# Kernel optimization log

Hardware: AMD Instinct MI355X
Metric: run time of the kernel (lower is better)

The kernel has to match this reference:

```python
import jax, jax.numpy as jnp
import numpy as np

B, C, T, N = 8, 64, 24, 512
H = 2
D = C // H  # 32
NEG = -1e9
LN_EPS = 1e-5


def setup_inputs() -> dict:
    key = jax.random.key(0)
    ks = jax.random.split(key, 8)
    s = 1.0 / np.sqrt(C)
    return {
        "x": jax.random.normal(ks[0], (B, C, T, N), jnp.float32),
        "gso": jax.random.randint(ks[1], (N, N), 0, 2, jnp.int32),
        "Wq": jax.random.normal(ks[2], (C, C), jnp.float32) * s,
        "Wk": jax.random.normal(ks[3], (C, C), jnp.float32) * s,
        "Wv": jax.random.normal(ks[4], (C, C), jnp.float32) * s,
        "a_src": jax.random.normal(ks[5], (H, D), jnp.float32) * s,
        "a_dst": jax.random.normal(ks[6], (H, D), jnp.float32) * s,
        "gamma": jnp.ones((C,), jnp.float32),
        "beta": jnp.zeros((C,), jnp.float32),
    }


def reference(x, gso, Wq, Wk, Wv, a_src, a_dst, gamma, beta):
    # x: (B, C, T, N) -> (M, N, C) with M = B*T
    xr = jnp.transpose(x, (0, 2, 3, 1)).reshape(B * T, N, C)
    # torch Linear: y = x @ W.T ; split heads -> (M, N, H, D)
    Q = jnp.einsum('mnc,dc->mnd', xr, Wq).reshape(B * T, N, H, D)
    K = jnp.einsum('mnc,dc->mnd', xr, Wk).reshape(B * T, N, H, D)
    V = jnp.einsum('mnc,dc->mnd', xr, Wv).reshape(B * T, N, H, D)
    # additive GAT scores: s_ij = leaky_relu(<q_i, a_src> + <k_j, a_dst>)
    s_src = jnp.einsum('mnhd,hd->mhn', Q, a_src)  # (M, H, N)
    s_dst = jnp.einsum('mnhd,hd->mhn', K, a_dst)  # (M, H, N)
    scores = s_src[:, :, :, None] + s_dst[:, :, None, :]  # (M, H, N, N)
    scores = jax.nn.leaky_relu(scores, negative_slope=0.2)
    mask = jnp.where(gso == 0, jnp.float32(NEG), jnp.float32(0.0))  # (N, N)
    scores = scores + mask[None, None, :, :]
    attn = jax.nn.softmax(scores, axis=-1)  # dropout is identity in eval
    out = jnp.einsum('mhij,mjhd->mihd', attn, V).reshape(B * T, N, C)
    # LayerNorm over channels
    mu = jnp.mean(out, axis=-1, keepdims=True)
    var = jnp.var(out, axis=-1, keepdims=True)
    out = (out - mu) * jax.lax.rsqrt(var + LN_EPS) * gamma + beta
    # (M, N, C) -> (B, C, T, N)
    return jnp.transpose(out.reshape(B, T, N, C), (0, 3, 1, 2))
```

## Files before the change

kernel.cpp:

```cpp
#include <hip/hip_runtime.h>


#define NB 8
#define NC 64
#define NT 24
#define NN 512
#define NM 192
#define LOG2E 1.44269504088896f
#define NEGBIG -1.0e9f

typedef float f32x4 __attribute__((ext_vector_type(4)));
typedef short bf16x8 __attribute__((ext_vector_type(8)));
typedef int   i32x4 __attribute__((ext_vector_type(4)));
typedef unsigned int u32;
typedef u32 u32x2 __attribute__((ext_vector_type(2)));

#ifndef __has_builtin
#define __has_builtin(x) 0
#endif

__device__ __forceinline__ float fast_exp2(float x) {
#if __has_builtin(__builtin_amdgcn_exp2f)
    return __builtin_amdgcn_exp2f(x);
#else
    return exp2f(x);
#endif
}

__device__ __forceinline__ unsigned short f2bf(float f) {
    union { float f; unsigned int u; } v; v.f = f;
    unsigned int u = v.u;
    u += 0x7fffu + ((u >> 16) & 1u);
    return (unsigned short)(u >> 16);
}

__device__ __forceinline__ float bf2f(unsigned short s) {
    union { unsigned int u; float f; } v;
    v.u = ((unsigned int)s) << 16;
    return v.f;
}

#define VT_IDX(h,k,qq,dt,dl,e) ((((((h)*16+(k))*4+(qq))*2+(dt))*16+(dl))*8+(e))

#define WS_VT_OFF   0u
#define WS_SSRC_OFF 12582912u
#define WS_SDST_OFF 13369344u
#define WS_MASK_OFF 14155776u
#define WS_NEEDED   15204352u

__global__ __launch_bounds__(512)
void gat_proj(const float* __restrict__ x, const int* __restrict__ gso,
              const float* __restrict__ Wq, const float* __restrict__ Wk,
              const float* __restrict__ Wv, const float* __restrict__ a_src,
              const float* __restrict__ a_dst,
              unsigned short* __restrict__ vt_ws, float* __restrict__ ssrc_ws,
              float* __restrict__ sdst_ws, float* __restrict__ mask_ws)
{
    __shared__ unsigned short sm_xrb[128][72];
    __shared__ unsigned short sm_wvb[4096];
    __shared__ float sm_wqa[2][NC];
    __shared__ float sm_wka[2][NC];

    const int bid  = blockIdx.x;
    const int m    = bid >> 2;
    const int ch   = bid & 3;
    const int b    = m / NT;
    const int tt   = m % NT;
    const int tid  = threadIdx.x;
    const int lane = tid & 63;
    const int wid  = tid >> 6;
    const int fr   = lane & 15;
    const int fq   = lane >> 4;

    if (bid < 16) {
        const int w  = bid * 512 + tid;
        const int i  = w >> 4, kk = w & 15;
        const int* gp = &gso[i * NN + kk * 32];
        float* mp = &mask_ws[i * NN + kk * 32];
        #pragma unroll
        for (int q = 0; q < 8; ++q) {
            const i32x4 g = *reinterpret_cast<const i32x4*>(gp + q * 4);
            f32x4 f;
            #pragma unroll
            for (int e = 0; e < 4; ++e) f[e] = (g[e] != 0) ? 0.f : NEGBIG;
            *reinterpret_cast<f32x4*>(mp + q * 4) = f;
        }
    }

    if (tid < 128) {
        const int h = tid >> 6, c = tid & 63;
        float aq = 0.f, ak = 0.f;
        #pragma unroll
        for (int d = 0; d < 32; ++d) {
            aq += Wq[(h*32 + d)*NC + c] * a_src[h*32 + d];
            ak += Wk[(h*32 + d)*NC + c] * a_dst[h*32 + d];
        }
        sm_wqa[h][c] = aq * LOG2E;
        sm_wka[h][c] = ak * LOG2E;
    }
    for (int idx = tid; idx < 4096; idx += 512) {
        const int e   = idx & 7;
        const int dl  = (idx >> 3) & 15;
        const int dt4 = (idx >> 7) & 3;
        const int qq  = (idx >> 9) & 3;
        const int ks  = idx >> 11;
        sm_wvb[idx] = f2bf(Wv[(dt4*16 + dl)*NC + ks*32 + qq*8 + e]);
    }
    __syncthreads();

    const int nl = tid >> 2;
    const int pp = tid & 3;
    const int nbase = ch * 128;

    #pragma unroll
    for (int half = 0; half < 2; ++half) {
        unsigned short tmp[8];
        #pragma unroll
        for (int e = 0; e < 8; ++e) {
            const int c = pp*16 + half*8 + e;
            tmp[e] = f2bf(x[((size_t)(b*NC + c)*NT + tt)*NN + nbase + nl]);
        }
        *reinterpret_cast<bf16x8*>(&sm_xrb[nl][pp*16 + half*8]) =
            *reinterpret_cast<const bf16x8*>(tmp);
    }
    __syncthreads();

    {
        float sq0=0.f, sq1=0.f, sk0=0.f, sk1=0.f;
        #pragma unroll
        for (int cc = 0; cc < 16; ++cc) {
            const int c = pp*16 + cc;
            const float xv = bf2f(sm_xrb[nl][c]);
            sq0 += xv * sm_wqa[0][c];
            sq1 += xv * sm_wqa[1][c];
            sk0 += xv * sm_wka[0][c];
            sk1 += xv * sm_wka[1][c];
        }
        sq0 += __shfl_xor(sq0,1); sq0 += __shfl_xor(sq0,2);
        sq1 += __shfl_xor(sq1,1); sq1 += __shfl_xor(sq1,2);
        sk0 += __shfl_xor(sk0,1); sk0 += __shfl_xor(sk0,2);
        sk1 += __shfl_xor(sk1,1); sk1 += __shfl_xor(sk1,2);
        if (pp == 0) {
            ssrc_ws[((size_t)m*2 + 0)*NN + nbase + nl] = sq0;
            ssrc_ws[((size_t)m*2 + 1)*NN + nbase + nl] = sq1;
            sdst_ws[((size_t)m*2 + 0)*NN + nbase + nl] = sk0;
            sdst_ws[((size_t)m*2 + 1)*NN + nbase + nl] = sk1;
        }
    }

    {
        f32x4 vacc[4] = {};
        #pragma unroll
        for (int ks = 0; ks < 2; ++ks) {
            const bf16x8 af = *reinterpret_cast<const bf16x8*>(
                &sm_xrb[wid*16 + fr][ks*32 + fq*8]);
            #pragma unroll
            for (int dt4 = 0; dt4 < 4; ++dt4) {
                const bf16x8 bfv = *reinterpret_cast<const bf16x8*>(
                    &sm_wvb[(((ks*4 + fq)*4 + dt4)*16 + fr)*8]);
                vacc[dt4] = __builtin_amdgcn_mfma_f32_16x16x32_bf16(
                    af, bfv, vacc[dt4], 0, 0, 0);
            }
        }
        const int n0 = nbase + wid*16 + 4*fq;
        #pragma unroll
        for (int dt4 = 0; dt4 < 4; ++dt4) {
            const int h = dt4 >> 1, dt = dt4 & 1;
            const u32 d0 = (u32)f2bf(vacc[dt4][0]) | ((u32)f2bf(vacc[dt4][1]) << 16);
            const u32 d1 = (u32)f2bf(vacc[dt4][2]) | ((u32)f2bf(vacc[dt4][3]) << 16);
            u32x2 dd; dd[0] = d0; dd[1] = d1;
            *reinterpret_cast<u32x2*>(
                &vt_ws[(size_t)m*32768 + VT_IDX(h, n0>>5, (n0>>3)&3, dt, fr, n0&7)]) = dd;
        }
    }
}

__global__ __launch_bounds__(512)
void gat_attn(const unsigned short* __restrict__ vt_ws,
              const float* __restrict__ ssrc_ws, const float* __restrict__ sdst_ws,
              const float* __restrict__ mask_ws,
              const float* __restrict__ gamma, const float* __restrict__ beta,
              float* __restrict__ out)
{
    __shared__ unsigned short sm_vt[32768];
    __shared__ float sm_sdst[2][NN];
    __shared__ float sm_ssrc[2][128];

    const int bid  = blockIdx.x;
    const int m    = bid >> 2;
    const int ch   = bid & 3;
    const int b    = m / NT;
    const int tt   = m % NT;
    const int tid  = threadIdx.x;
    const int lane = tid & 63;
    const int wid  = tid >> 6;
    const int fr   = lane & 15;
    const int fq   = lane >> 4;

    {
        const char* src = (const char*)(vt_ws + (size_t)m * 32768);
#if __has_builtin(__builtin_amdgcn_global_load_lds)
        #pragma unroll
        for (int i = 0; i < 8; ++i) {
            __builtin_amdgcn_global_load_lds(
                (const __attribute__((address_space(1))) void*)
                    (src + i*8192 + tid*16),
                (__attribute__((address_space(3))) void*)
                    (((__attribute__((address_space(3))) char*)sm_vt) +
                     i*8192 + (tid & ~63)*16),
                16, 0, 0);
        }
#else
        #pragma unroll
        for (int i = 0; i < 8; ++i) {
            reinterpret_cast<i32x4*>(sm_vt)[i*512 + tid] =
                reinterpret_cast<const i32x4*>(src)[i*512 + tid];
        }
#endif
    }
    if (tid < 256) {
        reinterpret_cast<f32x4*>(&sm_sdst[0][0])[tid] =
            reinterpret_cast<const f32x4*>(sdst_ws + (size_t)m*2*NN)[tid];
    } else {
        const int t = tid - 256;
        const int h = t >> 7, nloc = t & 127;
        sm_ssrc[h][nloc] = ssrc_ws[((size_t)m*2 + h)*NN + ch*128 + nloc];
    }
    __syncthreads();

    float gmv[4], btv[4];
    #pragma unroll
    for (int dt4 = 0; dt4 < 4; ++dt4) {
        gmv[dt4] = gamma[dt4*16 + fr];
        btv[dt4] = beta [dt4*16 + fr];
    }

    bf16x8 bones;
    {
        union { i32x4 i; bf16x8 h; } cv;
        const int w = (fr == 0) ? 0x3F803F80 : 0;
        cv.i[0] = w; cv.i[1] = w; cv.i[2] = w; cv.i[3] = w;
        bones = cv.h;
    }

    const int iloc = wid * 16;
    const int ig   = ch*128 + iloc + fr;
    const float src0 = sm_ssrc[0][iloc + fr];
    const float src1 = sm_ssrc[1][iloc + fr];

    f32x4 acc[4] = {};
    f32x4 accs0 = {}, accs1 = {};

    for (int k = 0; k < 16; ++k) {
        const int j0 = k*32 + fq*8;
        const float* mp = &mask_ws[(size_t)ig * NN + j0];
        const f32x4 ma = *reinterpret_cast<const f32x4*>(mp);
        const f32x4 mb = *reinterpret_cast<const f32x4*>(mp + 4);

        {
            const f32x4 da = *reinterpret_cast<const f32x4*>(&sm_sdst[0][j0]);
            const f32x4 db = *reinterpret_cast<const f32x4*>(&sm_sdst[0][j0+4]);
            u32 u[8];
            #pragma unroll
            for (int e = 0; e < 4; ++e) {
                float sc = src0 + da[e] + ma[e];
                sc = fmaxf(sc, 0.2f*sc);
                u[e] = __float_as_uint(fast_exp2(sc));
            }
            #pragma unroll
            for (int e = 0; e < 4; ++e) {
                float sc = src0 + db[e] + mb[e];
                sc = fmaxf(sc, 0.2f*sc);
                u[4+e] = __float_as_uint(fast_exp2(sc));
            }
            union { i32x4 i; bf16x8 h; } cv;
            cv.i[0] = __builtin_amdgcn_perm(u[1], u[0], 0x07060302u);
            cv.i[1] = __builtin_amdgcn_perm(u[3], u[2], 0x07060302u);
            cv.i[2] = __builtin_amdgcn_perm(u[5], u[4], 0x07060302u);
            cv.i[3] = __builtin_amdgcn_perm(u[7], u[6], 0x07060302u);
            const bf16x8 af = cv.h;
            accs0 = __builtin_amdgcn_mfma_f32_16x16x32_bf16(af, bones, accs0, 0,0,0);
            const bf16x8 b0 = *reinterpret_cast<const bf16x8*>(&sm_vt[VT_IDX(0,k,fq,0,fr,0)]);
            const bf16x8 b1 = *reinterpret_cast<const bf16x8*>(&sm_vt[VT_IDX(0,k,fq,1,fr,0)]);
            acc[0] = __builtin_amdgcn_mfma_f32_16x16x32_bf16(af, b0, acc[0], 0,0,0);
            acc[1] = __builtin_amdgcn_mfma_f32_16x16x32_bf16(af, b1, acc[1], 0,0,0);
        }
        {
            const f32x4 da = *reinterpret_cast<const f32x4*>(&sm_sdst[1][j0]);
            const f32x4 db = *reinterpret_cast<const f32x4*>(&sm_sdst[1][j0+4]);
            u32 u[8];
            #pragma unroll
            for (int e = 0; e < 4; ++e) {
                float sc = src1 + da[e] + ma[e];
                sc = fmaxf(sc, 0.2f*sc);
                u[e] = __float_as_uint(fast_exp2(sc));
            }
            #pragma unroll
            for (int e = 0; e < 4; ++e) {
                float sc = src1 + db[e] + mb[e];
                sc = fmaxf(sc, 0.2f*sc);
                u[4+e] = __float_as_uint(fast_exp2(sc));
            }
            union { i32x4 i; bf16x8 h; } cv;
            cv.i[0] = __builtin_amdgcn_perm(u[1], u[0], 0x07060302u);
            cv.i[1] = __builtin_amdgcn_perm(u[3], u[2], 0x07060302u);
            cv.i[2] = __builtin_amdgcn_perm(u[5], u[4], 0x07060302u);
            cv.i[3] = __builtin_amdgcn_perm(u[7], u[6], 0x07060302u);
            const bf16x8 af = cv.h;
            accs1 = __builtin_amdgcn_mfma_f32_16x16x32_bf16(af, bones, accs1, 0,0,0);
            const bf16x8 b0 = *reinterpret_cast<const bf16x8*>(&sm_vt[VT_IDX(1,k,fq,0,fr,0)]);
            const bf16x8 b1 = *reinterpret_cast<const bf16x8*>(&sm_vt[VT_IDX(1,k,fq,1,fr,0)]);
            acc[2] = __builtin_amdgcn_mfma_f32_16x16x32_bf16(af, b0, acc[2], 0,0,0);
            acc[3] = __builtin_amdgcn_mfma_f32_16x16x32_bf16(af, b1, acc[3], 0,0,0);
        }
    }

    #pragma unroll
    for (int rg = 0; rg < 4; ++rg) {
        const int rowloc = 4*fq + rg;
        const float rs0 = __shfl(accs0[rg], lane & 48);
        const float rs1 = __shfl(accs1[rg], lane & 48);
        const float inv0 = 1.f / rs0, inv1 = 1.f / rs1;
        float vv[4];
        vv[0] = acc[0][rg] * inv0;
        vv[1] = acc[1][rg] * inv0;
        vv[2] = acc[2][rg] * inv1;
        vv[3] = acc[3][rg] * inv1;
        float sum = vv[0]+vv[1]+vv[2]+vv[3];
        float ssq = vv[0]*vv[0]+vv[1]*vv[1]+vv[2]*vv[2]+vv[3]*vv[3];
        sum += __shfl_xor(sum,1); sum += __shfl_xor(sum,2);
        sum += __shfl_xor(sum,4); sum += __shfl_xor(sum,8);
        ssq += __shfl_xor(ssq,1); ssq += __shfl_xor(ssq,2);
        ssq += __shfl_xor(ssq,4); ssq += __shfl_xor(ssq,8);
        const float mu   = sum * (1.f/64.f);
        const float var  = ssq * (1.f/64.f) - mu*mu;
        const float rstd = rsqrtf(var + 1e-5f);
        const int irow = ch*128 + iloc + rowloc;
        #pragma unroll
        for (int dt4 = 0; dt4 < 4; ++dt4) {
            const float o = (vv[dt4] - mu) * rstd * gmv[dt4] + btv[dt4];
            out[((size_t)(b*NC + dt4*16 + fr)*NT + tt)*NN + irow] = o;
        }
    }
}

__global__ __launch_bounds__(512)
void gat_fused_mono(const float* __restrict__ x, const int* __restrict__ gso,
               const float* __restrict__ Wq, const float* __restrict__ Wk,
               const float* __restrict__ Wv, const float* __restrict__ a_src,
               const float* __restrict__ a_dst, const float* __restrict__ gamma,
               const float* __restrict__ beta, float* __restrict__ out)
{
    __shared__ unsigned short sm_xrb[128][72];
    __shared__ unsigned short sm_vt[32768];
    __shared__ unsigned short sm_wvb[4096];
    __shared__ float sm_ssrc[2][NN];
    __shared__ float sm_sdst[2][NN];
    __shared__ float sm_wqa[2][NC];
    __shared__ float sm_wka[2][NC];

    const int m    = blockIdx.x;
    const int b    = m / NT;
    const int tt   = m % NT;
    const int tid  = threadIdx.x;
    const int lane = tid & 63;
    const int wid  = tid >> 6;
    const int fr   = lane & 15;
    const int fq   = lane >> 4;

    if (tid < 128) {
        const int h = tid >> 6, c = tid & 63;
        float aq = 0.f, ak = 0.f;
        #pragma unroll
        for (int d = 0; d < 32; ++d) {
            aq += Wq[(h*32 + d)*NC + c] * a_src[h*32 + d];
            ak += Wk[(h*32 + d)*NC + c] * a_dst[h*32 + d];
        }
        sm_wqa[h][c] = aq;
        sm_wka[h][c] = ak;
    }
    for (int idx = tid; idx < 4096; idx += 512) {
        const int e   = idx & 7;
        const int dl  = (idx >> 3) & 15;
        const int dt4 = (idx >> 7) & 3;
        const int qq  = (idx >> 9) & 3;
        const int ks  = idx >> 11;
        sm_wvb[idx] = f2bf(Wv[(dt4*16 + dl)*NC + ks*32 + qq*8 + e]);
    }
    __syncthreads();

    const int nl = tid >> 2;
    const int pp = tid & 3;

    for (int ch = 0; ch < 4; ++ch) {
        const int nbase = ch * 128;
        #pragma unroll
        for (int half = 0; half < 2; ++half) {
            unsigned short tmp[8];
            #pragma unroll
            for (int e = 0; e < 8; ++e) {
                const int c = pp*16 + half*8 + e;
                tmp[e] = f2bf(x[((size_t)(b*NC + c)*NT + tt)*NN + nbase + nl]);
            }
            *reinterpret_cast<bf16x8*>(&sm_xrb[nl][pp*16 + half*8]) =
                *reinterpret_cast<const bf16x8*>(tmp);
        }
        __syncthreads();
        {
            float sq0=0.f, sq1=0.f, sk0=0.f, sk1=0.f;
            #pragma unroll
            for (int cc = 0; cc < 16; ++cc) {
                const int c = pp*16 + cc;
                const float xv = bf2f(sm_xrb[nl][c]);
                sq0 += xv * sm_wqa[0][c];
                sq1 += xv * sm_wqa[1][c];
                sk0 += xv * sm_wka[0][c];
                sk1 += xv * sm_wka[1][c];
            }
            sq0 += __shfl_xor(sq0,1); sq0 += __shfl_xor(sq0,2);
            sq1 += __shfl_xor(sq1,1); sq1 += __shfl_xor(sq1,2);
            sk0 += __shfl_xor(sk0,1); sk0 += __shfl_xor(sk0,2);
            sk1 += __shfl_xor(sk1,1); sk1 += __shfl_xor(sk1,2);
            if (pp == 0) {
                sm_ssrc[0][nbase+nl] = sq0;
                sm_ssrc[1][nbase+nl] = sq1;
                sm_sdst[0][nbase+nl] = sk0;
                sm_sdst[1][nbase+nl] = sk1;
            }
        }
        {
            f32x4 vacc[4] = {};
            #pragma unroll
            for (int ks = 0; ks < 2; ++ks) {
                const bf16x8 af = *reinterpret_cast<const bf16x8*>(
                    &sm_xrb[wid*16 + fr][ks*32 + fq*8]);
                #pragma unroll
                for (int dt4 = 0; dt4 < 4; ++dt4) {
                    const bf16x8 bfv = *reinterpret_cast<const bf16x8*>(
                        &sm_wvb[(((ks*4 + fq)*4 + dt4)*16 + fr)*8]);
                    vacc[dt4] = __builtin_amdgcn_mfma_f32_16x16x32_bf16(
                        af, bfv, vacc[dt4], 0, 0, 0);
                }
            }
            #pragma unroll
            for (int dt4 = 0; dt4 < 4; ++dt4) {
                const int h = dt4 >> 1, dt = dt4 & 1;
                #pragma unroll
                for (int rg = 0; rg < 4; ++rg) {
                    const int n = nbase + wid*16 + 4*fq + rg;
                    sm_vt[VT_IDX(h, n>>5, (n>>3)&3, dt, fr, n&7)] = f2bf(vacc[dt4][rg]);
                }
            }
        }
        __syncthreads();
    }

    float gmv[4], btv[4];
    #pragma unroll
    for (int dt4 = 0; dt4 < 4; ++dt4) {
        gmv[dt4] = gamma[dt4*16 + fr];
        btv[dt4] = beta [dt4*16 + fr];
    }

    for (int it = 0; it < 4; ++it) {
        const int ibase = (wid*4 + it) * 16;
        const int ig = ibase + fr;
        const float src0 = sm_ssrc[0][ig];
        const float src1 = sm_ssrc[1][ig];
        f32x4 acc[4] = {};
        float rsum0 = 0.f, rsum1 = 0.f;

        for (int k = 0; k < 16; ++k) {
            const int j0 = k*32 + fq*8;
            const int* gp = &gso[ig*NN + j0];
            const i32x4 g0 = *reinterpret_cast<const i32x4*>(gp);
            const i32x4 g1 = *reinterpret_cast<const i32x4*>(gp + 4);
            {
                const f32x4 da = *reinterpret_cast<const f32x4*>(&sm_sdst[0][j0]);
                const f32x4 db = *reinterpret_cast<const f32x4*>(&sm_sdst[0][j0+4]);
                bf16x8 af;
                #pragma unroll
                for (int e = 0; e < 4; ++e) {
                    float sc = src0 + da[e];
                    sc = fmaxf(sc, 0.2f*sc);
                    float ev = __expf(sc);
                    ev = (g0[e] != 0) ? ev : 0.f;
                    const unsigned short wb = f2bf(ev);
                    rsum0 += bf2f(wb);
                    af[e] = (short)wb;
                }
                #pragma unroll
                for (int e = 0; e < 4; ++e) {
                    float sc = src0 + db[e];
                    sc = fmaxf(sc, 0.2f*sc);
                    float ev = __expf(sc);
                    ev = (g1[e] != 0) ? ev : 0.f;
                    const unsigned short wb = f2bf(ev);
                    rsum0 += bf2f(wb);
                    af[4+e] = (short)wb;
                }
                const bf16x8 b0 = *reinterpret_cast<const bf16x8*>(&sm_vt[VT_IDX(0,k,fq,0,fr,0)]);
                const bf16x8 b1 = *reinterpret_cast<const bf16x8*>(&sm_vt[VT_IDX(0,k,fq,1,fr,0)]);
                acc[0] = __builtin_amdgcn_mfma_f32_16x16x32_bf16(af, b0, acc[0], 0,0,0);
                acc[1] = __builtin_amdgcn_mfma_f32_16x16x32_bf16(af, b1, acc[1], 0,0,0);
            }
            {
                const f32x4 da = *reinterpret_cast<const f32x4*>(&sm_sdst[1][j0]);
                const f32x4 db = *reinterpret_cast<const f32x4*>(&sm_sdst[1][j0+4]);
                bf16x8 af;
                #pragma unroll
                for (int e = 0; e < 4; ++e) {
                    float sc = src1 + da[e];
                    sc = fmaxf(sc, 0.2f*sc);
                    float ev = __expf(sc);
                    ev = (g0[e] != 0) ? ev : 0.f;
                    const unsigned short wb = f2bf(ev);
                    rsum1 += bf2f(wb);
                    af[e] = (short)wb;
                }
                #pragma unroll
                for (int e = 0; e < 4; ++e) {
                    float sc = src1 + db[e];
                    sc = fmaxf(sc, 0.2f*sc);
                    float ev = __expf(sc);
                    ev = (g1[e] != 0) ? ev : 0.f;
                    const unsigned short wb = f2bf(ev);
                    rsum1 += bf2f(wb);
                    af[4+e] = (short)wb;
                }
                const bf16x8 b0 = *reinterpret_cast<const bf16x8*>(&sm_vt[VT_IDX(1,k,fq,0,fr,0)]);
                const bf16x8 b1 = *reinterpret_cast<const bf16x8*>(&sm_vt[VT_IDX(1,k,fq,1,fr,0)]);
                acc[2] = __builtin_amdgcn_mfma_f32_16x16x32_bf16(af, b0, acc[2], 0,0,0);
                acc[3] = __builtin_amdgcn_mfma_f32_16x16x32_bf16(af, b1, acc[3], 0,0,0);
            }
        }

        rsum0 += __shfl_xor(rsum0, 16); rsum0 += __shfl_xor(rsum0, 32);
        rsum1 += __shfl_xor(rsum1, 16); rsum1 += __shfl_xor(rsum1, 32);

        #pragma unroll
        for (int rg = 0; rg < 4; ++rg) {
            const int rowloc   = 4*fq + rg;
            const int src_lane = (lane & 48) | rowloc;
            const float rs0 = __shfl(rsum0, src_lane);
            const float rs1 = __shfl(rsum1, src_lane);
            const float inv0 = 1.f / rs0, inv1 = 1.f / rs1;
            float vv[4];
            vv[0] = acc[0][rg] * inv0;
            vv[1] = acc[1][rg] * inv0;
            vv[2] = acc[2][rg] * inv1;
            vv[3] = acc[3][rg] * inv1;
            float sum = vv[0]+vv[1]+vv[2]+vv[3];
            float ssq = vv[0]*vv[0]+vv[1]*vv[1]+vv[2]*vv[2]+vv[3]*vv[3];
            sum += __shfl_xor(sum,1); sum += __shfl_xor(sum,2);
            sum += __shfl_xor(sum,4); sum += __shfl_xor(sum,8);
            ssq += __shfl_xor(ssq,1); ssq += __shfl_xor(ssq,2);
            ssq += __shfl_xor(ssq,4); ssq += __shfl_xor(ssq,8);
            const float mu   = sum * (1.f/64.f);
            const float var  = ssq * (1.f/64.f) - mu*mu;
            const float rstd = rsqrtf(var + 1e-5f);
            const int irow = ibase + rowloc;
            #pragma unroll
            for (int dt4 = 0; dt4 < 4; ++dt4) {
                const float o = (vv[dt4] - mu) * rstd * gmv[dt4] + btv[dt4];
                out[((size_t)(b*NC + dt4*16 + fr)*NT + tt)*NN + irow] = o;
            }
        }
    }
}

extern "C" void kernel_launch(void* const* d_in, const int* in_sizes, int n_in,
                              void* d_out, int out_size, void* d_ws, size_t ws_size,
                              hipStream_t stream) {
    (void)in_sizes; (void)n_in; (void)out_size;
    const float* x     = (const float*)d_in[0];
    const int*   gso   = (const int*)  d_in[1];
    const float* Wq    = (const float*)d_in[2];
    const float* Wk    = (const float*)d_in[3];
    const float* Wv    = (const float*)d_in[4];
    const float* a_src = (const float*)d_in[5];
    const float* a_dst = (const float*)d_in[6];
    const float* gamma = (const float*)d_in[7];
    const float* beta  = (const float*)d_in[8];
    float* out = (float*)d_out;

    if (ws_size >= (size_t)WS_NEEDED && d_ws != nullptr) {
        unsigned short* vt = (unsigned short*)((char*)d_ws + WS_VT_OFF);
        float* ssrc  = (float*)((char*)d_ws + WS_SSRC_OFF);
        float* sdst  = (float*)((char*)d_ws + WS_SDST_OFF);
        float* maskf = (float*)((char*)d_ws + WS_MASK_OFF);
        gat_proj<<<768, 512, 0, stream>>>(x, gso, Wq, Wk, Wv, a_src, a_dst,
                                          vt, ssrc, sdst, maskf);
        gat_attn<<<768, 512, 0, stream>>>(vt, ssrc, sdst, maskf, gamma, beta, out);
    } else {
        gat_fused_mono<<<NM, 512, 0, stream>>>(x, gso, Wq, Wk, Wv, a_src, a_dst,
                                               gamma, beta, out);
    }
}
```

Measured before the change: 56.16 us.

## Halve attention LDS footprint by streaming V in two chunks, swizzle x tile

Reorders the V workspace so each 32-column key chunk holds both heads contiguously. The attention kernel then loads only half of V into LDS at a time and reloads the second half midway, between barriers. This halves shared memory per block so more blocks can be resident per CU, at the cost of a mid-loop stall on the reload. The projection kernel's x tile gets an XOR swizzle against LDS bank conflicts, and the attention block index is remapped so consecutive blocks share mask rows for L2 reuse.

New measurement: 49.30 us. 1.14x faster.

```diff
diff --git a/kernel.cpp b/kernel.cpp
--- a/kernel.cpp
+++ b/kernel.cpp
@@ -39,6 +39,11 @@
     v.u = ((unsigned int)s) << 16;
     return v.f;
 }
+
+#define VT2_IDX(k2,h,qq,dt,dl,e) \
+    ((((((k2)*2+(h))*4+(qq))*2+(dt))*16+(dl))*8+(e))
+
+#define XRB(n,c) (((n)<<6) + (((((c)>>3) ^ ((n)&7))<<3) | ((c)&7)))
 
 #define VT_IDX(h,k,qq,dt,dl,e) ((((((h)*16+(k))*4+(qq))*2+(dt))*16+(dl))*8+(e))
 
@@ -56,7 +61,7 @@
               unsigned short* __restrict__ vt_ws, float* __restrict__ ssrc_ws,
               float* __restrict__ sdst_ws, float* __restrict__ mask_ws)
 {
-    __shared__ unsigned short sm_xrb[128][72];
+    __shared__ unsigned short sm_xrb[8192];
     __shared__ unsigned short sm_wvb[4096];
     __shared__ float sm_wqa[2][NC];
     __shared__ float sm_wka[2][NC];
@@ -106,31 +111,34 @@
         const int ks  = idx >> 11;
         sm_wvb[idx] = f2bf(Wv[(dt4*16 + dl)*NC + ks*32 + qq*8 + e]);
     }
+
+    const int nbase = ch * 128;
+
+    {
+        const int sl = tid & 127;
+        const int sc = tid >> 7;
+        #pragma unroll
+        for (int half = 0; half < 2; ++half) {
+            unsigned short tmp[8];
+            #pragma unroll
+            for (int e = 0; e < 8; ++e) {
+                const int c = sc*16 + half*8 + e;
+                tmp[e] = f2bf(x[((size_t)(b*NC + c)*NT + tt)*NN + nbase + sl]);
+            }
+            *reinterpret_cast<bf16x8*>(&sm_xrb[XRB(sl, sc*16 + half*8)]) =
+                *reinterpret_cast<const bf16x8*>(tmp);
+        }
+    }
     __syncthreads();
 
-    const int nl = tid >> 2;
-    const int pp = tid & 3;
-    const int nbase = ch * 128;
-
-    #pragma unroll
-    for (int half = 0; half < 2; ++half) {
-        unsigned short tmp[8];
-        #pragma unroll
-        for (int e = 0; e < 8; ++e) {
-            const int c = pp*16 + half*8 + e;
-            tmp[e] = f2bf(x[((size_t)(b*NC + c)*NT + tt)*NN + nbase + nl]);
-        }
-        *reinterpret_cast<bf16x8*>(&sm_xrb[nl][pp*16 + half*8]) =
-            *reinterpret_cast<const bf16x8*>(tmp);
-    }
-    __syncthreads();
-
     {
+        const int nl = tid >> 2;
+        const int pp = tid & 3;
         float sq0=0.f, sq1=0.f, sk0=0.f, sk1=0.f;
         #pragma unroll
         for (int cc = 0; cc < 16; ++cc) {
             const int c = pp*16 + cc;
-            const float xv = bf2f(sm_xrb[nl][c]);
+            const float xv = bf2f(sm_xrb[XRB(nl, c)]);
             sq0 += xv * sm_wqa[0][c];
             sq1 += xv * sm_wqa[1][c];
             sk0 += xv * sm_wka[0][c];
@@ -153,7 +161,7 @@
         #pragma unroll
         for (int ks = 0; ks < 2; ++ks) {
             const bf16x8 af = *reinterpret_cast<const bf16x8*>(
-                &sm_xrb[wid*16 + fr][ks*32 + fq*8]);
+                &sm_xrb[XRB(wid*16 + fr, ks*32 + fq*8)]);
             #pragma unroll
             for (int dt4 = 0; dt4 < 4; ++dt4) {
                 const bf16x8 bfv = *reinterpret_cast<const bf16x8*>(
@@ -170,7 +178,8 @@
             const u32 d1 = (u32)f2bf(vacc[dt4][2]) | ((u32)f2bf(vacc[dt4][3]) << 16);
             u32x2 dd; dd[0] = d0; dd[1] = d1;
             *reinterpret_cast<u32x2*>(
-                &vt_ws[(size_t)m*32768 + VT_IDX(h, n0>>5, (n0>>3)&3, dt, fr, n0&7)]) = dd;
+                &vt_ws[(size_t)m*32768 +
+                       VT2_IDX(n0>>5, h, (n0>>3)&3, dt, fr, n0&7)]) = dd;
         }
     }
 }
@@ -182,13 +191,13 @@
               const float* __restrict__ gamma, const float* __restrict__ beta,
               float* __restrict__ out)
 {
-    __shared__ unsigned short sm_vt[32768];
+    __shared__ unsigned short sm_vt[16384];
     __shared__ float sm_sdst[2][NN];
     __shared__ float sm_ssrc[2][128];
 
     const int bid  = blockIdx.x;
-    const int m    = bid >> 2;
-    const int ch   = bid & 3;
+    const int m    = (bid >> 5) * 8 + (bid & 7);
+    const int ch   = (bid >> 3) & 3;
     const int b    = m / NT;
     const int tt   = m % NT;
     const int tid  = threadIdx.x;
@@ -197,27 +206,25 @@
     const int fr   = lane & 15;
     const int fq   = lane >> 4;
 
-    {
-        const char* src = (const char*)(vt_ws + (size_t)m * 32768);
+    const char* vsrc = (const char*)(vt_ws + (size_t)m * 32768);
 #if __has_builtin(__builtin_amdgcn_global_load_lds)
-        #pragma unroll
-        for (int i = 0; i < 8; ++i) {
-            __builtin_amdgcn_global_load_lds(
-                (const __attribute__((address_space(1))) void*)
-                    (src + i*8192 + tid*16),
-                (__attribute__((address_space(3))) void*)
-                    (((__attribute__((address_space(3))) char*)sm_vt) +
-                     i*8192 + (tid & ~63)*16),
-                16, 0, 0);
-        }
+    #pragma unroll
+    for (int i = 0; i < 4; ++i) {
+        __builtin_amdgcn_global_load_lds(
+            (const __attribute__((address_space(1))) void*)
+                (vsrc + i*8192 + tid*16),
+            (__attribute__((address_space(3))) void*)
+                (((__attribute__((address_space(3))) char*)sm_vt) +
+                 i*8192 + (tid & ~63)*16),
+            16, 0, 0);
+    }
 #else
-        #pragma unroll
-        for (int i = 0; i < 8; ++i) {
-            reinterpret_cast<i32x4*>(sm_vt)[i*512 + tid] =
-                reinterpret_cast<const i32x4*>(src)[i*512 + tid];
-        }
+    #pragma unroll
+    for (int i = 0; i < 4; ++i) {
+        reinterpret_cast<i32x4*>(sm_vt)[i*512 + tid] =
+            reinterpret_cast<const i32x4*>(vsrc)[i*512 + tid];
+    }
 #endif
-    }
     if (tid < 256) {
         reinterpret_cast<f32x4*>(&sm_sdst[0][0])[tid] =
             reinterpret_cast<const f32x4*>(sdst_ws + (size_t)m*2*NN)[tid];
@@ -247,71 +254,103 @@
     const int ig   = ch*128 + iloc + fr;
     const float src0 = sm_ssrc[0][iloc + fr];
     const float src1 = sm_ssrc[1][iloc + fr];
+    const float* mrow = mask_ws + (size_t)ig * NN;
 
     f32x4 acc[4] = {};
     f32x4 accs0 = {}, accs1 = {};
 
-    for (int k = 0; k < 16; ++k) {
-        const int j0 = k*32 + fq*8;
-        const float* mp = &mask_ws[(size_t)ig * NN + j0];
-        const f32x4 ma = *reinterpret_cast<const f32x4*>(mp);
-        const f32x4 mb = *reinterpret_cast<const f32x4*>(mp + 4);
-
-        {
-            const f32x4 da = *reinterpret_cast<const f32x4*>(&sm_sdst[0][j0]);
-            const f32x4 db = *reinterpret_cast<const f32x4*>(&sm_sdst[0][j0+4]);
-            u32 u[8];
-            #pragma unroll
-            for (int e = 0; e < 4; ++e) {
-                float sc = src0 + da[e] + ma[e];
-                sc = fmaxf(sc, 0.2f*sc);
-                u[e] = __float_as_uint(fast_exp2(sc));
-            }
-            #pragma unroll
-            for (int e = 0; e < 4; ++e) {
-                float sc = src0 + db[e] + mb[e];
-                sc = fmaxf(sc, 0.2f*sc);
-                u[4+e] = __float_as_uint(fast_exp2(sc));
-            }
-            union { i32x4 i; bf16x8 h; } cv;
-            cv.i[0] = __builtin_amdgcn_perm(u[1], u[0], 0x07060302u);
-            cv.i[1] = __builtin_amdgcn_perm(u[3], u[2], 0x07060302u);
-            cv.i[2] = __builtin_amdgcn_perm(u[5], u[4], 0x07060302u);
-            cv.i[3] = __builtin_amdgcn_perm(u[7], u[6], 0x07060302u);
-            const bf16x8 af = cv.h;
-            accs0 = __builtin_amdgcn_mfma_f32_16x16x32_bf16(af, bones, accs0, 0,0,0);
-            const bf16x8 b0 = *reinterpret_cast<const bf16x8*>(&sm_vt[VT_IDX(0,k,fq,0,fr,0)]);
-            const bf16x8 b1 = *reinterpret_cast<const bf16x8*>(&sm_vt[VT_IDX(0,k,fq,1,fr,0)]);
-            acc[0] = __builtin_amdgcn_mfma_f32_16x16x32_bf16(af, b0, acc[0], 0,0,0);
-            acc[1] = __builtin_amdgcn_mfma_f32_16x16x32_bf16(af, b1, acc[1], 0,0,0);
-        }
-        {
-            const f32x4 da = *reinterpret_cast<const f32x4*>(&sm_sdst[1][j0]);
-            const f32x4 db = *reinterpret_cast<const f32x4*>(&sm_sdst[1][j0+4]);
-            u32 u[8];
-            #pragma unroll
-            for (int e = 0; e < 4; ++e) {
-                float sc = src1 + da[e] + ma[e];
-                sc = fmaxf(sc, 0.2f*sc);
-                u[e] = __float_as_uint(fast_exp2(sc));
-            }
-            #pragma unroll
-            for (int e = 0; e < 4; ++e) {
-                float sc = src1 + db[e] + mb[e];
-                sc = fmaxf(sc, 0.2f*sc);
-                u[4+e] = __float_as_uint(fast_exp2(sc));
-            }
-            union { i32x4 i; bf16x8 h; } cv;
-            cv.i[0] = __builtin_amdgcn_perm(u[1], u[0], 0x07060302u);
-            cv.i[1] = __builtin_amdgcn_perm(u[3], u[2], 0x07060302u);
-            cv.i[2] = __builtin_amdgcn_perm(u[5], u[4], 0x07060302u);
-            cv.i[3] = __builtin_amdgcn_perm(u[7], u[6], 0x07060302u);
-            const bf16x8 af = cv.h;
-            accs1 = __builtin_amdgcn_mfma_f32_16x16x32_bf16(af, bones, accs1, 0,0,0);
-            const bf16x8 b0 = *reinterpret_cast<const bf16x8*>(&sm_vt[VT_IDX(1,k,fq,0,fr,0)]);
-            const bf16x8 b1 = *reinterpret_cast<const bf16x8*>(&sm_vt[VT_IDX(1,k,fq,1,fr,0)]);
-            acc[2] = __builtin_amdgcn_mfma_f32_16x16x32_bf16(af, b0, acc[2], 0,0,0);
-            acc[3] = __builtin_amdgcn_mfma_f32_16x16x32_bf16(af, b1, acc[3], 0,0,0);
+    #pragma unroll
+    for (int hf = 0; hf < 2; ++hf) {
+        for (int k2 = 0; k2 < 8; ++k2) {
+            const int k  = hf*8 + k2;
+            const int j0 = k*32 + fq*8;
+            const float* mp = mrow + j0;
+            const f32x4 ma = *reinterpret_cast<const f32x4*>(mp);
+            const f32x4 mb = *reinterpret_cast<const f32x4*>(mp + 4);
+
+            {
+                const f32x4 da = *reinterpret_cast<const f32x4*>(&sm_sdst[0][j0]);
+                const f32x4 db = *reinterpret_cast<const f32x4*>(&sm_sdst[0][j0+4]);
+                u32 u[8];
+                #pragma unroll
+                for (int e = 0; e < 4; ++e) {
+                    float sc = src0 + da[e] + ma[e];
+                    sc = fmaxf(sc, 0.2f*sc);
+                    u[e] = __float_as_uint(fast_exp2(sc));
+                }
+                #pragma unroll
+                for (int e = 0; e < 4; ++e) {
+                    float sc = src0 + db[e] + mb[e];
+                    sc = fmaxf(sc, 0.2f*sc);
+                    u[4+e] = __float_as_uint(fast_exp2(sc));
+                }
+                union { i32x4 i; bf16x8 h; } cv;
+                cv.i[0] = __builtin_amdgcn_perm(u[1], u[0], 0x07060302u);
+                cv.i[1] = __builtin_amdgcn_perm(u[3], u[2], 0x07060302u);
+                cv.i[2] = __builtin_amdgcn_perm(u[5], u[4], 0x07060302u);
+                cv.i[3] = __builtin_amdgcn_perm(u[7], u[6], 0x07060302u);
+                const bf16x8 af = cv.h;
+                accs0 = __builtin_amdgcn_mfma_f32_16x16x32_bf16(af, bones, accs0, 0,0,0);
+                const bf16x8 b0 = *reinterpret_cast<const bf16x8*>(
+                    &sm_vt[VT2_IDX(k2,0,fq,0,fr,0)]);
+                const bf16x8 b1 = *reinterpret_cast<const bf16x8*>(
+                    &sm_vt[VT2_IDX(k2,0,fq,1,fr,0)]);
+                acc[0] = __builtin_amdgcn_mfma_f32_16x16x32_bf16(af, b0, acc[0], 0,0,0);
+                acc[1] = __builtin_amdgcn_mfma_f32_16x16x32_bf16(af, b1, acc[1], 0,0,0);
+            }
+            {
+                const f32x4 da = *reinterpret_cast<const f32x4*>(&sm_sdst[1][j0]);
+                const f32x4 db = *reinterpret_cast<const f32x4*>(&sm_sdst[1][j0+4]);
+                u32 u[8];
+                #pragma unroll
+                for (int e = 0; e < 4; ++e) {
+                    float sc = src1 + da[e] + ma[e];
+                    sc = fmaxf(sc, 0.2f*sc);
+                    u[e] = __float_as_uint(fast_exp2(sc));
+                }
+                #pragma unroll
+                for (int e = 0; e < 4; ++e) {
+                    float sc = src1 + db[e] + mb[e];
+                    sc = fmaxf(sc, 0.2f*sc);
+                    u[4+e] = __float_as_uint(fast_exp2(sc));
+                }
+                union { i32x4 i; bf16x8 h; } cv;
+                cv.i[0] = __builtin_amdgcn_perm(u[1], u[0], 0x07060302u);
+                cv.i[1] = __builtin_amdgcn_perm(u[3], u[2], 0x07060302u);
+                cv.i[2] = __builtin_amdgcn_perm(u[5], u[4], 0x07060302u);
+                cv.i[3] = __builtin_amdgcn_perm(u[7], u[6], 0x07060302u);
+                const bf16x8 af = cv.h;
+                accs1 = __builtin_amdgcn_mfma_f32_16x16x32_bf16(af, bones, accs1, 0,0,0);
+                const bf16x8 b0 = *reinterpret_cast<const bf16x8*>(
+                    &sm_vt[VT2_IDX(k2,1,fq,0,fr,0)]);
+                const bf16x8 b1 = *reinterpret_cast<const bf16x8*>(
+                    &sm_vt[VT2_IDX(k2,1,fq,1,fr,0)]);
+                acc[2] = __builtin_amdgcn_mfma_f32_16x16x32_bf16(af, b0, acc[2], 0,0,0);
+                acc[3] = __builtin_amdgcn_mfma_f32_16x16x32_bf16(af, b1, acc[3], 0,0,0);
+            }
+        }
+
+        if (hf == 0) {
+            __syncthreads();
+#if __has_builtin(__builtin_amdgcn_global_load_lds)
+            #pragma unroll
+            for (int i = 0; i < 4; ++i) {
+                __builtin_amdgcn_global_load_lds(
+                    (const __attribute__((address_space(1))) void*)
+                        (vsrc + 32768 + i*8192 + tid*16),
+                    (__attribute__((address_space(3))) void*)
+                        (((__attribute__((address_space(3))) char*)sm_vt) +
+                         i*8192 + (tid & ~63)*16),
+                    16, 0, 0);
+            }
+#else
+            #pragma unroll
+            for (int i = 0; i < 4; ++i) {
+                reinterpret_cast<i32x4*>(sm_vt)[i*512 + tid] =
+                    reinterpret_cast<const i32x4*>(vsrc + 32768)[i*512 + tid];
+            }
+#endif
+            __syncthreads();
         }
     }
 
```
